# Kernel tuning notes

Measured on AMD Instinct MI355X. Metric: run time of the kernel, lower is better.

The kernel has to match this reference:

```python
import jax, jax.numpy as jnp
import numpy as np

N_NODES = 100000
N_EDGES = 1600000
F_IN = 5
F_HID = 64
F_OUT = 72
NEG_SLOPE = 0.2  # PyG GATConv default


def setup_inputs() -> dict:
    key = jax.random.key(0)
    ks = jax.random.split(key, 8)
    x = jax.random.normal(ks[0], (N_NODES, F_IN), dtype=jnp.float32)
    edge_index = jax.random.randint(ks[1], (2, N_EDGES), 0, N_NODES, dtype=jnp.int64)
    # GATConv params (heads=1, concat=True)
    W = jax.random.normal(ks[2], (F_IN, F_HID), dtype=jnp.float32) * (1.0 / np.sqrt(F_IN))
    att_src = jax.random.normal(ks[3], (F_HID,), dtype=jnp.float32) * (1.0 / np.sqrt(F_HID))
    att_dst = jax.random.normal(ks[4], (F_HID,), dtype=jnp.float32) * (1.0 / np.sqrt(F_HID))
    b_gat = jnp.zeros((F_HID,), dtype=jnp.float32)
    # feature_extractor: Linear(64 -> 72) + ReLU
    W_fc = jax.random.normal(ks[5], (F_HID, F_OUT), dtype=jnp.float32) * (1.0 / np.sqrt(F_HID))
    b_fc = jnp.zeros((F_OUT,), dtype=jnp.float32)
    return {"x": x, "edge_index": edge_index, "W": W, "att_src": att_src,
            "att_dst": att_dst, "b_gat": b_gat, "W_fc": W_fc, "b_fc": b_fc}


def _gat_forward(x, edge_index, W, att_src, att_dst, b_gat, W_fc, b_fc):
    N = x.shape[0]
    h = x @ W  # [N, F_HID]
    # add self loops (PyG GATConv default add_self_loops=True)
    loops = jnp.arange(N, dtype=edge_index.dtype)
    src = jnp.concatenate([edge_index[0], loops])  # [E + N]
    dst = jnp.concatenate([edge_index[1], loops])
    # per-node attention halves, gathered per edge
    a_s = h @ att_src  # [N]
    a_d = h @ att_dst  # [N]
    e = a_s[src] + a_d[dst]  # [E + N]
    e = jnp.where(e > 0, e, NEG_SLOPE * e)  # LeakyReLU
    # edge-softmax grouped by destination node
    m = jax.ops.segment_max(e, dst, num_segments=N)  # self loops => no empty segment
    ex = jnp.exp(e - m[dst])
    denom = jax.ops.segment_sum(ex, dst, num_segments=N)
    alpha = ex / (denom[dst] + 1e-16)
    # weighted scatter-add aggregation
    out = jax.ops.segment_sum(alpha[:, None] * h[src], dst, num_segments=N) + b_gat  # [N, F_HID]
    pooled = jnp.mean(out, axis=0, keepdims=True)  # [1, F_HID]
    return jax.nn.relu(pooled @ W_fc + b_fc)  # [1, F_OUT]


def reference(x, edge_index, W, att_src, att_dst, b_gat, W_fc, b_fc):
    return _gat_forward(x, edge_index, W, att_src, att_dst, b_gat, W_fc, b_fc)
```

## Files before the change

### kernel.cpp

```cpp
#include <hip/hip_runtime.h>


#define NR 25
#define RSHIFT 12
#define RSZ 4096
#define RMASK 4095
#define BBIN 256
#define BINTHR 1024
#define T 8
#define POOLX_BLOCKS 32

__global__ __launch_bounds__(256) void k_att(
    const float* __restrict__ x, const float* __restrict__ W,
    const float* __restrict__ att_src, const float* __restrict__ att_dst,
    float* __restrict__ a_s, float* __restrict__ a_d, int N) {
  const int lane = threadIdx.x & 63;
  const int n = blockIdx.x * 4 + (threadIdx.x >> 6);
  if (n >= N) return;
  const float x0 = x[n * 5 + 0], x1 = x[n * 5 + 1], x2 = x[n * 5 + 2],
              x3 = x[n * 5 + 3], x4 = x[n * 5 + 4];
  float hv = x0 * W[0 * 64 + lane];
  hv += x1 * W[1 * 64 + lane];
  hv += x2 * W[2 * 64 + lane];
  hv += x3 * W[3 * 64 + lane];
  hv += x4 * W[4 * 64 + lane];
  float t1 = hv * att_src[lane];
  float t2 = hv * att_dst[lane];
#pragma unroll
  for (int o = 32; o > 0; o >>= 1) {
    t1 += __shfl_xor(t1, o, 64);
    t2 += __shfl_xor(t2, o, 64);
  }
  if (lane == 0) {
    a_s[n] = t1;
    a_d[n] = t2;
  }
}

__global__ __launch_bounds__(BINTHR) void k_count(
    const int* __restrict__ ei, int* __restrict__ counts_d,
    int* __restrict__ counts_s, int E) {
  __shared__ int cd[NR], cs[NR];
  if (threadIdx.x < NR) {
    cd[threadIdx.x] = 0;
    cs[threadIdx.x] = 0;
  }
  __syncthreads();
  const int chunk = (E + BBIN - 1) / BBIN;
  const int lo = blockIdx.x * chunk;
  const int hi = (lo + chunk < E) ? lo + chunk : E;
#pragma unroll 4
  for (int j = lo + threadIdx.x; j < hi; j += BINTHR) {
    atomicAdd(&cs[ei[j] >> RSHIFT], 1);
    atomicAdd(&cd[ei[E + j] >> RSHIFT], 1);
  }
  __syncthreads();
  if (threadIdx.x < NR) {
    counts_d[threadIdx.x * BBIN + blockIdx.x] = cd[threadIdx.x];
    counts_s[threadIdx.x * BBIN + blockIdx.x] = cs[threadIdx.x];
  }
}

__global__ __launch_bounds__(BINTHR) void k_scan(
    const int* __restrict__ counts_d, const int* __restrict__ counts_s,
    int* __restrict__ offs_d, int* __restrict__ offs_s,
    int* __restrict__ rinfo) {
  __shared__ int lc[2 * NR * BBIN];
  __shared__ int tot[2 * NR];
  __shared__ int base[2 * NR];
  for (int i = threadIdx.x; i < 2 * NR * BBIN; i += BINTHR)
    lc[i] = (i < NR * BBIN) ? counts_d[i] : counts_s[i - NR * BBIN];
  __syncthreads();
  if (threadIdx.x < 2 * NR) {
    int s = 0;
    const int* row = &lc[threadIdx.x * BBIN];
    for (int b = 0; b < BBIN; ++b) s += row[b];
    tot[threadIdx.x] = s;
  }
  __syncthreads();
  if (threadIdx.x == 0) {
    int a = 0;
    for (int r = 0; r < NR; ++r) {
      base[r] = a;
      a += tot[r];
    }
    a = 0;
    for (int r = 0; r < NR; ++r) {
      base[NR + r] = a;
      a += tot[NR + r];
    }
  }
  __syncthreads();
  if (threadIdx.x < 2 * NR) {
    int run = base[threadIdx.x];
    int* orow = (threadIdx.x < NR) ? &offs_d[threadIdx.x * BBIN]
                                   : &offs_s[(threadIdx.x - NR) * BBIN];
    const int* row = &lc[threadIdx.x * BBIN];
    for (int b = 0; b < BBIN; ++b) {
      orow[b] = run;
      run += row[b];
    }
  }
  if (threadIdx.x < NR) {
    rinfo[0 * NR + threadIdx.x] = base[threadIdx.x];
    rinfo[1 * NR + threadIdx.x] = tot[threadIdx.x];
    rinfo[2 * NR + threadIdx.x] = base[NR + threadIdx.x];
    rinfo[3 * NR + threadIdx.x] = tot[NR + threadIdx.x];
  }
}

__global__ __launch_bounds__(BINTHR) void k_scatter(
    const int* __restrict__ ei, const float* __restrict__ a_s,
    const float* __restrict__ a_d, const int* __restrict__ offs_d,
    const int* __restrict__ offs_s, uint2* __restrict__ rec_d,
    uint2* __restrict__ rec_s, int E) {
  __shared__ int curd[NR], curs[NR];
  if (threadIdx.x < NR) {
    curd[threadIdx.x] = offs_d[threadIdx.x * BBIN + blockIdx.x];
    curs[threadIdx.x] = offs_s[threadIdx.x * BBIN + blockIdx.x];
  }
  __syncthreads();
  const int chunk = (E + BBIN - 1) / BBIN;
  const int lo = blockIdx.x * chunk;
  const int hi = (lo + chunk < E) ? lo + chunk : E;
#pragma unroll 2
  for (int j = lo + threadIdx.x; j < hi; j += BINTHR) {
    const int s = ei[j];
    const int d = ei[E + j];
    float e = a_s[s] + a_d[d];
    e = e > 0.f ? e : 0.2f * e;
    const float ex = __expf(e);
    const int sd = atomicAdd(&curd[d >> RSHIFT], 1);
    rec_d[sd] = make_uint2((unsigned)(d & RMASK), __float_as_uint(ex));
    const int ss = atomicAdd(&curs[s >> RSHIFT], 1);
    rec_s[ss] = make_uint2((unsigned)(s & RMASK) | ((unsigned)d << RSHIFT),
                           __float_as_uint(ex));
  }
}

template <int PASS>
__global__ __launch_bounds__(256) void k_hist(
    const uint2* __restrict__ rec, const int* __restrict__ rinfo,
    const float* __restrict__ rden, float* __restrict__ slab) {
  __shared__ float hist[RSZ];
  const int r = blockIdx.x / T;
  const int t = blockIdx.x % T;
  for (int i = threadIdx.x; i < RSZ; i += 256) hist[i] = 0.f;
  __syncthreads();
  const int base = rinfo[(PASS == 1 ? 0 : 2) * NR + r];
  const int tot = rinfo[(PASS == 1 ? 1 : 3) * NR + r];
  const int L = (tot + T - 1) / T;
  const int lo = base + t * L;
  const int hh = (t + 1) * L < tot ? (t + 1) * L : tot;
  const int hi = base + hh;
#pragma unroll 4
  for (int j = lo + threadIdx.x; j < hi; j += 256) {
    const uint2 rv = rec[j];
    float v = __uint_as_float(rv.y);
    unsigned ki;
    if (PASS == 1) {
      ki = rv.x;
    } else {
      ki = rv.x & RMASK;
      v *= rden[rv.x >> RSHIFT];
    }
    atomicAdd(&hist[ki], v);
  }
  __syncthreads();
  float* outp = slab + ((size_t)(r * T + t)) * RSZ;
  for (int i = threadIdx.x; i < RSZ; i += 256) outp[i] = hist[i];
}

template <int PASS>
__global__ __launch_bounds__(256) void k_red(
    const float* __restrict__ slab, const float* __restrict__ a_s,
    const float* __restrict__ a_d, const float* __restrict__ rden_in,
    float* __restrict__ outarr, int N) {
  const int n = blockIdx.x * 256 + threadIdx.x;
  if (n >= N) return;
  const int g = n >> RSHIFT;
  const int i = n & RMASK;
  const float* sp = slab + (size_t)g * T * RSZ + i;
  float sum = 0.f;
#pragma unroll
  for (int t = 0; t < T; ++t) sum += sp[(size_t)t * RSZ];
  float e = a_s[n] + a_d[n];
  e = e > 0.f ? e : 0.2f * e;
  const float ex_self = __expf(e);
  if (PASS == 1)
    outarr[n] = 1.0f / (sum + ex_self + 1e-16f);
  else
    outarr[n] = sum + ex_self * rden_in[n];
}

__global__ __launch_bounds__(256) void k_poolx(
    const float* __restrict__ x, const float* __restrict__ c,
    float* __restrict__ partial, int N) {
  float a0 = 0.f, a1 = 0.f, a2 = 0.f, a3 = 0.f, a4 = 0.f;
  for (int n = blockIdx.x * 256 + threadIdx.x; n < N; n += gridDim.x * 256) {
    const float cv = c[n];
    const float* xp = x + (size_t)n * 5;
    a0 += cv * xp[0];
    a1 += cv * xp[1];
    a2 += cv * xp[2];
    a3 += cv * xp[3];
    a4 += cv * xp[4];
  }
#pragma unroll
  for (int o = 32; o > 0; o >>= 1) {
    a0 += __shfl_xor(a0, o, 64);
    a1 += __shfl_xor(a1, o, 64);
    a2 += __shfl_xor(a2, o, 64);
    a3 += __shfl_xor(a3, o, 64);
    a4 += __shfl_xor(a4, o, 64);
  }
  __shared__ float s5[4][5];
  const int lane = threadIdx.x & 63;
  const int w = threadIdx.x >> 6;
  if (lane == 0) {
    s5[w][0] = a0;
    s5[w][1] = a1;
    s5[w][2] = a2;
    s5[w][3] = a3;
    s5[w][4] = a4;
  }
  __syncthreads();
  if (threadIdx.x < 5)
    partial[blockIdx.x * 5 + threadIdx.x] =
        s5[0][threadIdx.x] + s5[1][threadIdx.x] + s5[2][threadIdx.x] +
        s5[3][threadIdx.x];
}

__global__ __launch_bounds__(256) void k_finish(
    const float* __restrict__ partial, const float* __restrict__ W,
    const float* __restrict__ b_gat, const float* __restrict__ W_fc,
    const float* __restrict__ b_fc, float* __restrict__ out, float invN) {
  __shared__ float pp[POOLX_BLOCKS * 5];
  __shared__ float px[5];
  __shared__ float pooled[64];
  const int t = threadIdx.x;
  if (t < POOLX_BLOCKS * 5) pp[t] = partial[t];
  __syncthreads();
  if (t < 5) {
    float s = 0.f;
    for (int b = 0; b < POOLX_BLOCKS; ++b) s += pp[b * 5 + t];
    px[t] = s * invN;
  }
  __syncthreads();
  if (t < 64) {
    float s = b_gat[t];
#pragma unroll
    for (int k = 0; k < 5; ++k) s += px[k] * W[k * 64 + t];
    pooled[t] = s;
  }
  __syncthreads();
  if (t < 72) {
    float s = b_fc[t];
#pragma unroll
    for (int f = 0; f < 64; ++f) s += pooled[f] * W_fc[f * 72 + t];
    out[t] = s > 0.f ? s : 0.f;
  }
}

extern "C" void kernel_launch(void* const* d_in, const int* in_sizes, int n_in,
                              void* d_out, int out_size, void* d_ws,
                              size_t ws_size, hipStream_t stream) {
  const float* x = (const float*)d_in[0];
  const int* ei = (const int*)d_in[1];
  const float* W = (const float*)d_in[2];
  const float* att_src = (const float*)d_in[3];
  const float* att_dst = (const float*)d_in[4];
  const float* b_gat = (const float*)d_in[5];
  const float* W_fc = (const float*)d_in[6];
  const float* b_fc = (const float*)d_in[7];
  float* out = (float*)d_out;

  const int N = in_sizes[0] / 5;
  const int E = in_sizes[1] / 2;

  char* p = (char*)d_ws;
  auto alloc = [&](size_t nbytes) -> void* {
    void* r = (void*)p;
    p += (nbytes + 255) & ~(size_t)255;
    return r;
  };
  float* a_s = (float*)alloc((size_t)N * sizeof(float));
  float* a_d = (float*)alloc((size_t)N * sizeof(float));
  float* rden = (float*)alloc((size_t)N * sizeof(float));
  float* c = (float*)alloc((size_t)N * sizeof(float));
  int* counts_d = (int*)alloc((size_t)NR * BBIN * sizeof(int));
  int* counts_s = (int*)alloc((size_t)NR * BBIN * sizeof(int));
  int* offs_d = (int*)alloc((size_t)NR * BBIN * sizeof(int));
  int* offs_s = (int*)alloc((size_t)NR * BBIN * sizeof(int));
  int* rinfo = (int*)alloc((size_t)4 * NR * sizeof(int));
  uint2* rec_d = (uint2*)alloc((size_t)E * sizeof(uint2));
  uint2* rec_s = (uint2*)alloc((size_t)E * sizeof(uint2));
  float* slab = (float*)alloc((size_t)NR * T * RSZ * sizeof(float));
  float* partial = (float*)alloc((size_t)POOLX_BLOCKS * 5 * sizeof(float));

  k_att<<<(N + 3) / 4, 256, 0, stream>>>(x, W, att_src, att_dst, a_s, a_d, N);
  k_count<<<BBIN, BINTHR, 0, stream>>>(ei, counts_d, counts_s, E);
  k_scan<<<1, BINTHR, 0, stream>>>(counts_d, counts_s, offs_d, offs_s, rinfo);
  k_scatter<<<BBIN, BINTHR, 0, stream>>>(ei, a_s, a_d, offs_d, offs_s, rec_d,
                                         rec_s, E);
  k_hist<1><<<NR * T, 256, 0, stream>>>(rec_d, rinfo, nullptr, slab);
  k_red<1><<<(N + 255) / 256, 256, 0, stream>>>(slab, a_s, a_d, nullptr, rden,
                                                N);
  k_hist<2><<<NR * T, 256, 0, stream>>>(rec_s, rinfo, rden, slab);
  k_red<2><<<(N + 255) / 256, 256, 0, stream>>>(slab, a_s, a_d, rden, c, N);
  k_poolx<<<POOLX_BLOCKS, 256, 0, stream>>>(x, c, partial, N);
  k_finish<<<1, 256, 0, stream>>>(partial, W, b_gat, W_fc, b_fc, out,
                                  1.0f / (float)N);
}
```

Measured before the change: 167.5 us.

## Replace source-binned second pass with direct per-edge weighted pooling of x

```diff
diff --git a/kernel.cpp b/kernel.cpp
--- a/kernel.cpp
+++ b/kernel.cpp
@@ -8,7 +8,7 @@
 #define BBIN 256
 #define BINTHR 1024
 #define T 8
-#define POOLX_BLOCKS 32
+#define PXE_BLOCKS 512
 
 __global__ __launch_bounds__(256) void k_att(
     const float* __restrict__ x, const float* __restrict__ W,
@@ -37,41 +37,31 @@
   }
 }
 
-__global__ __launch_bounds__(BINTHR) void k_count(
-    const int* __restrict__ ei, int* __restrict__ counts_d,
-    int* __restrict__ counts_s, int E) {
-  __shared__ int cd[NR], cs[NR];
-  if (threadIdx.x < NR) {
-    cd[threadIdx.x] = 0;
-    cs[threadIdx.x] = 0;
-  }
+__global__ __launch_bounds__(BINTHR) void k_cnt(const int* __restrict__ ei,
+                                                int* __restrict__ counts,
+                                                int E) {
+  __shared__ int cd[NR];
+  if (threadIdx.x < NR) cd[threadIdx.x] = 0;
   __syncthreads();
   const int chunk = (E + BBIN - 1) / BBIN;
   const int lo = blockIdx.x * chunk;
   const int hi = (lo + chunk < E) ? lo + chunk : E;
 #pragma unroll 4
-  for (int j = lo + threadIdx.x; j < hi; j += BINTHR) {
-    atomicAdd(&cs[ei[j] >> RSHIFT], 1);
+  for (int j = lo + threadIdx.x; j < hi; j += BINTHR)
     atomicAdd(&cd[ei[E + j] >> RSHIFT], 1);
-  }
+  __syncthreads();
+  if (threadIdx.x < NR)
+    counts[threadIdx.x * BBIN + blockIdx.x] = cd[threadIdx.x];
+}
+
+__global__ __launch_bounds__(BINTHR) void k_scan1(const int* __restrict__ counts,
+                                                  int* __restrict__ offs,
+                                                  int* __restrict__ rinfo) {
+  __shared__ int lc[NR * BBIN];
+  __shared__ int tot[NR], base[NR];
+  for (int i = threadIdx.x; i < NR * BBIN; i += BINTHR) lc[i] = counts[i];
   __syncthreads();
   if (threadIdx.x < NR) {
-    counts_d[threadIdx.x * BBIN + blockIdx.x] = cd[threadIdx.x];
-    counts_s[threadIdx.x * BBIN + blockIdx.x] = cs[threadIdx.x];
-  }
-}
-
-__global__ __launch_bounds__(BINTHR) void k_scan(
-    const int* __restrict__ counts_d, const int* __restrict__ counts_s,
-    int* __restrict__ offs_d, int* __restrict__ offs_s,
-    int* __restrict__ rinfo) {
-  __shared__ int lc[2 * NR * BBIN];
-  __shared__ int tot[2 * NR];
-  __shared__ int base[2 * NR];
-  for (int i = threadIdx.x; i < 2 * NR * BBIN; i += BINTHR)
-    lc[i] = (i < NR * BBIN) ? counts_d[i] : counts_s[i - NR * BBIN];
-  __syncthreads();
-  if (threadIdx.x < 2 * NR) {
     int s = 0;
     const int* row = &lc[threadIdx.x * BBIN];
     for (int b = 0; b < BBIN; ++b) s += row[b];
@@ -84,41 +74,28 @@
       base[r] = a;
       a += tot[r];
     }
-    a = 0;
-    for (int r = 0; r < NR; ++r) {
-      base[NR + r] = a;
-      a += tot[NR + r];
-    }
-  }
-  __syncthreads();
-  if (threadIdx.x < 2 * NR) {
+  }
+  __syncthreads();
+  if (threadIdx.x < NR) {
     int run = base[threadIdx.x];
-    int* orow = (threadIdx.x < NR) ? &offs_d[threadIdx.x * BBIN]
-                                   : &offs_s[(threadIdx.x - NR) * BBIN];
+    int* orow = &offs[threadIdx.x * BBIN];
     const int* row = &lc[threadIdx.x * BBIN];
     for (int b = 0; b < BBIN; ++b) {
       orow[b] = run;
       run += row[b];
     }
-  }
-  if (threadIdx.x < NR) {
-    rinfo[0 * NR + threadIdx.x] = base[threadIdx.x];
-    rinfo[1 * NR + threadIdx.x] = tot[threadIdx.x];
-    rinfo[2 * NR + threadIdx.x] = base[NR + threadIdx.x];
-    rinfo[3 * NR + threadIdx.x] = tot[NR + threadIdx.x];
-  }
-}
-
-__global__ __launch_bounds__(BINTHR) void k_scatter(
+    rinfo[threadIdx.x] = base[threadIdx.x];
+    rinfo[NR + threadIdx.x] = tot[threadIdx.x];
+  }
+}
+
+__global__ __launch_bounds__(BINTHR) void k_scat(
     const int* __restrict__ ei, const float* __restrict__ a_s,
-    const float* __restrict__ a_d, const int* __restrict__ offs_d,
-    const int* __restrict__ offs_s, uint2* __restrict__ rec_d,
-    uint2* __restrict__ rec_s, int E) {
-  __shared__ int curd[NR], curs[NR];
-  if (threadIdx.x < NR) {
-    curd[threadIdx.x] = offs_d[threadIdx.x * BBIN + blockIdx.x];
-    curs[threadIdx.x] = offs_s[threadIdx.x * BBIN + blockIdx.x];
-  }
+    const float* __restrict__ a_d, const int* __restrict__ offs,
+    uint2* __restrict__ rec, int E) {
+  __shared__ int cur[NR];
+  if (threadIdx.x < NR)
+    cur[threadIdx.x] = offs[threadIdx.x * BBIN + blockIdx.x];
   __syncthreads();
   const int chunk = (E + BBIN - 1) / BBIN;
   const int lo = blockIdx.x * chunk;
@@ -130,25 +107,21 @@
     float e = a_s[s] + a_d[d];
     e = e > 0.f ? e : 0.2f * e;
     const float ex = __expf(e);
-    const int sd = atomicAdd(&curd[d >> RSHIFT], 1);
-    rec_d[sd] = make_uint2((unsigned)(d & RMASK), __float_as_uint(ex));
-    const int ss = atomicAdd(&curs[s >> RSHIFT], 1);
-    rec_s[ss] = make_uint2((unsigned)(s & RMASK) | ((unsigned)d << RSHIFT),
-                           __float_as_uint(ex));
-  }
-}
-
-template <int PASS>
-__global__ __launch_bounds__(256) void k_hist(
-    const uint2* __restrict__ rec, const int* __restrict__ rinfo,
-    const float* __restrict__ rden, float* __restrict__ slab) {
+    const int slot = atomicAdd(&cur[d >> RSHIFT], 1);
+    rec[slot] = make_uint2((unsigned)(d & RMASK), __float_as_uint(ex));
+  }
+}
+
+__global__ __launch_bounds__(256) void k_hist(const uint2* __restrict__ rec,
+                                              const int* __restrict__ rinfo,
+                                              float* __restrict__ slab) {
   __shared__ float hist[RSZ];
   const int r = blockIdx.x / T;
   const int t = blockIdx.x % T;
   for (int i = threadIdx.x; i < RSZ; i += 256) hist[i] = 0.f;
   __syncthreads();
-  const int base = rinfo[(PASS == 1 ? 0 : 2) * NR + r];
-  const int tot = rinfo[(PASS == 1 ? 1 : 3) * NR + r];
+  const int base = rinfo[r];
+  const int tot = rinfo[NR + r];
   const int L = (tot + T - 1) / T;
   const int lo = base + t * L;
   const int hh = (t + 1) * L < tot ? (t + 1) * L : tot;
@@ -156,26 +129,17 @@
 #pragma unroll 4
   for (int j = lo + threadIdx.x; j < hi; j += 256) {
     const uint2 rv = rec[j];
-    float v = __uint_as_float(rv.y);
-    unsigned ki;
-    if (PASS == 1) {
-      ki = rv.x;
-    } else {
-      ki = rv.x & RMASK;
-      v *= rden[rv.x >> RSHIFT];
-    }
-    atomicAdd(&hist[ki], v);
+    atomicAdd(&hist[rv.x], __uint_as_float(rv.y));
   }
   __syncthreads();
   float* outp = slab + ((size_t)(r * T + t)) * RSZ;
   for (int i = threadIdx.x; i < RSZ; i += 256) outp[i] = hist[i];
 }
 
-template <int PASS>
-__global__ __launch_bounds__(256) void k_red(
-    const float* __restrict__ slab, const float* __restrict__ a_s,
-    const float* __restrict__ a_d, const float* __restrict__ rden_in,
-    float* __restrict__ outarr, int N) {
+__global__ __launch_bounds__(256) void k_rden(const float* __restrict__ slab,
+                                              const float* __restrict__ a_s,
+                                              const float* __restrict__ a_d,
+                                              float* __restrict__ rden, int N) {
   const int n = blockIdx.x * 256 + threadIdx.x;
   if (n >= N) return;
   const int g = n >> RSHIFT;
@@ -186,25 +150,37 @@
   for (int t = 0; t < T; ++t) sum += sp[(size_t)t * RSZ];
   float e = a_s[n] + a_d[n];
   e = e > 0.f ? e : 0.2f * e;
-  const float ex_self = __expf(e);
-  if (PASS == 1)
-    outarr[n] = 1.0f / (sum + ex_self + 1e-16f);
-  else
-    outarr[n] = sum + ex_self * rden_in[n];
-}
-
-__global__ __launch_bounds__(256) void k_poolx(
-    const float* __restrict__ x, const float* __restrict__ c,
-    float* __restrict__ partial, int N) {
+  rden[n] = 1.0f / (sum + __expf(e) + 1e-16f);
+}
+
+__global__ __launch_bounds__(256) void k_pxe(
+    const int* __restrict__ ei, const float* __restrict__ a_s,
+    const float* __restrict__ a_d, const float* __restrict__ rden,
+    const float* __restrict__ x, float* __restrict__ partial, int E, int N) {
   float a0 = 0.f, a1 = 0.f, a2 = 0.f, a3 = 0.f, a4 = 0.f;
+  for (int j = blockIdx.x * 256 + threadIdx.x; j < E; j += gridDim.x * 256) {
+    const int s = ei[j];
+    const int d = ei[E + j];
+    float e = a_s[s] + a_d[d];
+    e = e > 0.f ? e : 0.2f * e;
+    const float w = __expf(e) * rden[d];
+    const float* xp = x + (size_t)s * 5;
+    a0 += w * xp[0];
+    a1 += w * xp[1];
+    a2 += w * xp[2];
+    a3 += w * xp[3];
+    a4 += w * xp[4];
+  }
   for (int n = blockIdx.x * 256 + threadIdx.x; n < N; n += gridDim.x * 256) {
-    const float cv = c[n];
+    float e = a_s[n] + a_d[n];
+    e = e > 0.f ? e : 0.2f * e;
+    const float w = __expf(e) * rden[n];
     const float* xp = x + (size_t)n * 5;
-    a0 += cv * xp[0];
-    a1 += cv * xp[1];
-    a2 += cv * xp[2];
-    a3 += cv * xp[3];
-    a4 += cv * xp[4];
+    a0 += w * xp[0];
+    a1 += w * xp[1];
+    a2 += w * xp[2];
+    a3 += w * xp[3];
+    a4 += w * xp[4];
   }
 #pragma unroll
   for (int o = 32; o > 0; o >>= 1) {
@@ -231,19 +207,19 @@
         s5[3][threadIdx.x];
 }
 
-__global__ __launch_bounds__(256) void k_finish(
+__global__ __launch_bounds__(256) void k_fin(
     const float* __restrict__ partial, const float* __restrict__ W,
     const float* __restrict__ b_gat, const float* __restrict__ W_fc,
     const float* __restrict__ b_fc, float* __restrict__ out, float invN) {
-  __shared__ float pp[POOLX_BLOCKS * 5];
+  __shared__ float pp[PXE_BLOCKS * 5];
   __shared__ float px[5];
   __shared__ float pooled[64];
   const int t = threadIdx.x;
-  if (t < POOLX_BLOCKS * 5) pp[t] = partial[t];
+  for (int i = t; i < PXE_BLOCKS * 5; i += 256) pp[i] = partial[i];
   __syncthreads();
   if (t < 5) {
     float s = 0.f;
-    for (int b = 0; b < POOLX_BLOCKS; ++b) s += pp[b * 5 + t];
+    for (int b = 0; b < PXE_BLOCKS; ++b) s += pp[b * 5 + t];
     px[t] = s * invN;
   }
   __syncthreads();
@@ -287,28 +263,20 @@
   float* a_s = (float*)alloc((size_t)N * sizeof(float));
   float* a_d = (float*)alloc((size_t)N * sizeof(float));
   float* rden = (float*)alloc((size_t)N * sizeof(float));
-  float* c = (float*)alloc((size_t)N * sizeof(float));
-  int* counts_d = (int*)alloc((size_t)NR * BBIN * sizeof(int));
-  int* counts_s = (int*)alloc((size_t)NR * BBIN * sizeof(int));
-  int* offs_d = (int*)alloc((size_t)NR * BBIN * sizeof(int));
-  int* offs_s = (int*)alloc((size_t)NR * BBIN * sizeof(int));
-  int* rinfo = (int*)alloc((size_t)4 * NR * sizeof(int));
-  uint2* rec_d = (uint2*)alloc((size_t)E * sizeof(uint2));
-  uint2* rec_s = (uint2*)alloc((size_t)E * sizeof(uint2));
+  int* counts = (int*)alloc((size_t)NR * BBIN * sizeof(int));
+  int* offs = (int*)alloc((size_t)NR * BBIN * sizeof(int));
+  int* rinfo = (int*)alloc((size_t)2 * NR * sizeof(int));
+  uint2* rec = (uint2*)alloc((size_t)E * sizeof(uint2));
   float* slab = (float*)alloc((size_t)NR * T * RSZ * sizeof(float));
-  float* partial = (float*)alloc((size_t)POOLX_BLOCKS * 5 * sizeof(float));
+  float* partial = (float*)alloc((size_t)PXE_BLOCKS * 5 * sizeof(float));
 
   k_att<<<(N + 3) / 4, 256, 0, stream>>>(x, W, att_src, att_dst, a_s, a_d, N);
-  k_count<<<BBIN, BINTHR, 0, stream>>>(ei, counts_d, counts_s, E);
-  k_scan<<<1, BINTHR, 0, stream>>>(counts_d, counts_s, offs_d, offs_s, rinfo);
-  k_scatter<<<BBIN, BINTHR, 0, stream>>>(ei, a_s, a_d, offs_d, offs_s, rec_d,
-                                         rec_s, E);
-  k_hist<1><<<NR * T, 256, 0, stream>>>(rec_d, rinfo, nullptr, slab);
-  k_red<1><<<(N + 255) / 256, 256, 0, stream>>>(slab, a_s, a_d, nullptr, rden,
-                                                N);
-  k_hist<2><<<NR * T, 256, 0, stream>>>(rec_s, rinfo, rden, slab);
-  k_red<2><<<(N + 255) / 256, 256, 0, stream>>>(slab, a_s, a_d, rden, c, N);
-  k_poolx<<<POOLX_BLOCKS, 256, 0, stream>>>(x, c, partial, N);
-  k_finish<<<1, 256, 0, stream>>>(partial, W, b_gat, W_fc, b_fc, out,
-                                  1.0f / (float)N);
-}
+  k_cnt<<<BBIN, BINTHR, 0, stream>>>(ei, counts, E);
+  k_scan1<<<1, BINTHR, 0, stream>>>(counts, offs, rinfo);
+  k_scat<<<BBIN, BINTHR, 0, stream>>>(ei, a_s, a_d, offs, rec, E);
+  k_hist<<<NR * T, 256, 0, stream>>>(rec, rinfo, slab);
+  k_rden<<<(N + 255) / 256, 256, 0, stream>>>(slab, a_s, a_d, rden, N);
+  k_pxe<<<PXE_BLOCKS, 256, 0, stream>>>(ei, a_s, a_d, rden, x, partial, E, N);
+  k_fin<<<1, 256, 0, stream>>>(partial, W, b_gat, W_fc, b_fc, out,
+                               1.0f / (float)N);
+}
```

After: 168.1 us. No clear change (+0.3%).
